# Optimization experiments

Measured on AMD Instinct MI355X. Metric: run time of the kernel, lower is better.

Reference implementation:

```python
import jax, jax.numpy as jnp
import numpy as np

NEG_INF = -1e30


def setup_inputs() -> dict:
    key = jax.random.key(0)
    k1, k2, k3, k4, k5, k6 = jax.random.split(key, 6)
    B, CL, QL, H = 16, 512, 64, 768
    c = jax.random.normal(k1, (B, CL, H), dtype=jnp.float32)
    q = jax.random.normal(k2, (B, QL, H), dtype=jnp.float32)
    c_mask = jax.random.randint(k3, (B, CL), 0, 2, dtype=jnp.int32)
    q_mask = jax.random.randint(k4, (B, QL), 0, 2, dtype=jnp.int32)
    W = jax.random.normal(k5, (H, H), dtype=jnp.float32) * (1.0 / np.sqrt(H))
    b = jax.random.normal(k6, (H,), dtype=jnp.float32) * 0.01
    return {"c": c, "q": q, "c_mask": c_mask, "q_mask": q_mask, "W": W, "b": b}


def reference(c, q, c_mask, q_mask, W, b):
    # c: [B, CL, H], q: [B, QL, H]
    cm = c_mask.astype(bool)[:, :, None]   # [B, CL, 1]
    qm = q_mask.astype(bool)[:, None, :]   # [B, 1, QL]
    # projected context then similarity matrix s: [B, CL, QL]
    cp = jnp.einsum('bch,dh->bcd', c, W) + b
    s = jnp.einsum('bcd,bqd->bcq', cp, q)
    # dual masked softmax (c2q over query dim, q2c over context dim)
    s1 = jax.nn.softmax(jnp.where(qm, s, NEG_INF), axis=2)  # [B, CL, QL]
    s2 = jax.nn.softmax(jnp.where(cm, s, NEG_INF), axis=1)  # [B, CL, QL]
    # a = s1 @ q : context-to-query attention
    a = jnp.einsum('bcq,bqh->bch', s1, q)
    # bvec = (s1 @ s2^T) @ c : query-to-context attention
    ss = jnp.einsum('bcq,bdq->bcd', s1, s2)  # [B, CL, CL]
    bvec = jnp.einsum('bcd,bdh->bch', ss, c)
    x = jnp.concatenate([c, a, c * a, c * bvec], axis=2)  # [B, CL, 4H]
    return x
```

## Files before the change

kernel.cpp:

```cpp
#include <hip/hip_runtime.h>
#include <math.h>


#define B_  16
#define CL_ 512
#define QL_ 64
#define H_  768
#define M_  (B_ * CL_)

typedef __attribute__((ext_vector_type(8))) short s8v;
typedef __attribute__((ext_vector_type(4))) float f4v;

__device__ __forceinline__ unsigned short bf16_rne(float x) {
    unsigned int u = __float_as_uint(x);
    u += 0x7fffu + ((u >> 16) & 1u);
    return (unsigned short)(u >> 16);
}
__device__ __forceinline__ float bf16_f(unsigned short h) {
    return __uint_as_float((unsigned int)h << 16);
}
__device__ __forceinline__ void split2(float x, unsigned short& h, unsigned short& l) {
    h = bf16_rne(x);
    l = bf16_rne(x - bf16_f(h));
}

__global__ __launch_bounds__(256) void k_u_beta(const float* __restrict__ q,
    const float* __restrict__ W, const float* __restrict__ bias,
    unsigned short* __restrict__ uh, unsigned short* __restrict__ ul,
    float* __restrict__ beta)
{
    if (blockIdx.x >= 192) {
        const int row = (blockIdx.x - 192) * 4 + (threadIdx.x >> 6);
        const int lane = threadIdx.x & 63;
        float p = 0.f;
        for (int d = lane; d < H_; d += 64) p = fmaf(bias[d], q[(size_t)row * H_ + d], p);
#pragma unroll
        for (int o = 32; o; o >>= 1) p += __shfl_xor(p, o);
        if (lane == 0) beta[row] = p;
        return;
    }
    __shared__ unsigned short Wh[64][40], Wl[64][40];
    const int m0 = (blockIdx.x & 15) * 64, n0 = (blockIdx.x >> 4) * 64;
    const int t = threadIdx.x, w = t >> 6, lane = t & 63;
    const int fm = lane & 15, quad = lane >> 4;
    const int mrow = m0 + w * 16 + fm;
    const int dd = t >> 3, hc = (t & 7) * 8;
    f4v acc[4];
#pragma unroll
    for (int j = 0; j < 4; ++j) acc[j] = (f4v){0.f, 0.f, 0.f, 0.f};
    for (int k0 = 0; k0 < H_; k0 += 32) {
        const float* wp = &W[(size_t)(k0 + dd) * H_ + n0 + hc];
        const float4 v0 = *(const float4*)wp, v1 = *(const float4*)(wp + 4);
        const float* ap = &q[(size_t)mrow * H_ + k0 + quad * 8];
        const float4 a0 = *(const float4*)ap, a1 = *(const float4*)(ap + 4);
        const float as[8] = {a0.x, a0.y, a0.z, a0.w, a1.x, a1.y, a1.z, a1.w};
        s8v fah, fal;
#pragma unroll
        for (int j = 0; j < 8; ++j) { unsigned short h, l; split2(as[j], h, l); fah[j] = (short)h; fal[j] = (short)l; }
        const float ws[8] = {v0.x, v0.y, v0.z, v0.w, v1.x, v1.y, v1.z, v1.w};
        __syncthreads();
#pragma unroll
        for (int j = 0; j < 8; ++j) {
            unsigned short h, l; split2(ws[j], h, l);
            Wh[hc + j][dd] = h; Wl[hc + j][dd] = l;
        }
        __syncthreads();
#pragma unroll
        for (int tn = 0; tn < 4; ++tn) {
            const s8v bh = *(const s8v*)&Wh[tn * 16 + fm][quad * 8];
            const s8v bl = *(const s8v*)&Wl[tn * 16 + fm][quad * 8];
            acc[tn] = __builtin_amdgcn_mfma_f32_16x16x32_bf16(fah, bh, acc[tn], 0, 0, 0);
            acc[tn] = __builtin_amdgcn_mfma_f32_16x16x32_bf16(fah, bl, acc[tn], 0, 0, 0);
            acc[tn] = __builtin_amdgcn_mfma_f32_16x16x32_bf16(fal, bh, acc[tn], 0, 0, 0);
        }
    }
#pragma unroll
    for (int tn = 0; tn < 4; ++tn) {
        const int col = n0 + tn * 16 + fm;
#pragma unroll
        for (int r = 0; r < 4; ++r) {
            const int row = m0 + w * 16 + quad * 4 + r;
            unsigned short h, l; split2(acc[tn][r], h, l);
            uh[(size_t)row * H_ + col] = h;
            ul[(size_t)row * H_ + col] = l;
        }
    }
}

__global__ __launch_bounds__(256) void k_s_sm(const float* __restrict__ c,
    const unsigned short* __restrict__ uh, const unsigned short* __restrict__ ul,
    const float* __restrict__ beta, const int* __restrict__ q_mask,
    float* __restrict__ s, unsigned short* __restrict__ s1)
{
    __shared__ float sL[32][65];
    const int m0 = blockIdx.x * 32;
    const int batch = m0 >> 9;
    const int t = threadIdx.x, w = t >> 6, lane = t & 63;
    const int fm = lane & 15, quad = lane >> 4;
    const int msub = (w >> 1) * 16, ntile0 = (w & 1) * 2;
    const int mrow = m0 + msub + fm;
    f4v acc[2];
    acc[0] = (f4v){0.f, 0.f, 0.f, 0.f}; acc[1] = acc[0];
    for (int k0 = 0; k0 < H_; k0 += 32) {
        const float* ap = &c[(size_t)mrow * H_ + k0 + quad * 8];
        const float4 a0 = *(const float4*)ap, a1 = *(const float4*)(ap + 4);
        const float xs[8] = {a0.x, a0.y, a0.z, a0.w, a1.x, a1.y, a1.z, a1.w};
        s8v fah, fal;
#pragma unroll
        for (int j = 0; j < 8; ++j) { unsigned short h, l; split2(xs[j], h, l); fah[j] = (short)h; fal[j] = (short)l; }
#pragma unroll
        for (int i = 0; i < 2; ++i) {
            const int tn = ntile0 + i;
            const size_t bo = (size_t)(batch * QL_ + tn * 16 + fm) * H_ + k0 + quad * 8;
            const s8v bh = *(const s8v*)&uh[bo];
            const s8v bl = *(const s8v*)&ul[bo];
            acc[i] = __builtin_amdgcn_mfma_f32_16x16x32_bf16(fah, bh, acc[i], 0, 0, 0);
            acc[i] = __builtin_amdgcn_mfma_f32_16x16x32_bf16(fah, bl, acc[i], 0, 0, 0);
            acc[i] = __builtin_amdgcn_mfma_f32_16x16x32_bf16(fal, bh, acc[i], 0, 0, 0);
        }
    }
#pragma unroll
    for (int i = 0; i < 2; ++i) {
        const int col = (ntile0 + i) * 16 + fm;
        const float bb = beta[batch * QL_ + col];
#pragma unroll
        for (int r = 0; r < 4; ++r) {
            const int lr = msub + quad * 4 + r;
            const float v = acc[i][r] + bb;
            s[(size_t)(m0 + lr) * QL_ + col] = v;
            sL[lr][col] = v;
        }
    }
    __syncthreads();
    const bool qm = q_mask[batch * QL_ + lane] != 0;
#pragma unroll
    for (int rr = 0; rr < 8; ++rr) {
        const int lr = w * 8 + rr;
        const float x = qm ? sL[lr][lane] : -1e30f;
        float mx = x;
#pragma unroll
        for (int o = 32; o; o >>= 1) mx = fmaxf(mx, __shfl_xor(mx, o));
        const float e = __expf(x - mx);
        float sm = e;
#pragma unroll
        for (int o = 32; o; o >>= 1) sm += __shfl_xor(sm, o);
        s1[(size_t)(m0 + lr) * QL_ + lane] = bf16_rne(e / sm);
    }
}

__global__ __launch_bounds__(256) void k_sm_cols(const float* __restrict__ s,
    const int* __restrict__ c_mask, unsigned short* __restrict__ s2t)
{
    __shared__ float red[4];
    const int b = blockIdx.x >> 6, qi = blockIdx.x & 63;
    const int t = threadIdx.x;
    const float* sb = s + (size_t)b * CL_ * QL_ + qi;
    const int* cm = c_mask + b * CL_;
    float x0 = cm[t] ? sb[(size_t)t * QL_] : -1e30f;
    float x1 = cm[t + 256] ? sb[(size_t)(t + 256) * QL_] : -1e30f;
    float m = fmaxf(x0, x1);
#pragma unroll
    for (int o = 32; o; o >>= 1) m = fmaxf(m, __shfl_xor(m, o));
    if ((t & 63) == 0) red[t >> 6] = m;
    __syncthreads();
    m = fmaxf(fmaxf(red[0], red[1]), fmaxf(red[2], red[3]));
    __syncthreads();
    float e0 = __expf(x0 - m), e1 = __expf(x1 - m);
    float sm = e0 + e1;
#pragma unroll
    for (int o = 32; o; o >>= 1) sm += __shfl_xor(sm, o);
    if ((t & 63) == 0) red[t >> 6] = sm;
    __syncthreads();
    sm = red[0] + red[1] + red[2] + red[3];
    float inv = 1.f / sm;
    unsigned short* o = s2t + ((size_t)b * QL_ + qi) * CL_;
    o[t]       = bf16_rne(e0 * inv);
    o[t + 256] = bf16_rne(e1 * inv);
}

__global__ __launch_bounds__(256) void k_tfin(const unsigned short* __restrict__ s2t,
    const unsigned short* __restrict__ s1, const float* __restrict__ q,
    const float* __restrict__ c, float* __restrict__ out)
{
    __shared__ unsigned short Bs[64][40];
    __shared__ unsigned short qT[64][72];
    __shared__ unsigned short tT[64][72];
    const int h0 = blockIdx.x * 64;
    const int c0 = blockIdx.y * 256;
    const int b  = blockIdx.z;
    const int t = threadIdx.x, w = t >> 6, lane = t & 63;
    const int fm = lane & 15, quad = lane >> 4;

    {
        const int r = t >> 4, c4 = (t & 15) * 4;
#pragma unroll
        for (int i = 0; i < 4; ++i) {
            const int qr = r + 16 * i;
            const float4 v = *(const float4*)&q[((size_t)b * QL_ + qr) * H_ + h0 + c4];
            qT[c4 + 0][qr] = bf16_rne(v.x);
            qT[c4 + 1][qr] = bf16_rne(v.y);
            qT[c4 + 2][qr] = bf16_rne(v.z);
            qT[c4 + 3][qr] = bf16_rne(v.w);
        }
    }

    {
        const int dd = t >> 3, hc = (t & 7) * 8;
        f4v acc[4];
#pragma unroll
        for (int j = 0; j < 4; ++j) acc[j] = (f4v){0.f, 0.f, 0.f, 0.f};
        for (int d0 = 0; d0 < CL_; d0 += 32) {
            const float* cp = &c[((size_t)b * CL_ + d0 + dd) * H_ + h0 + hc];
            const float4 v0 = *(const float4*)cp, v1 = *(const float4*)(cp + 4);
            const float xs[8] = {v0.x, v0.y, v0.z, v0.w, v1.x, v1.y, v1.z, v1.w};
            __syncthreads();
#pragma unroll
            for (int j = 0; j < 8; ++j) Bs[hc + j][dd] = bf16_rne(xs[j]);
            __syncthreads();
            const s8v fb = *(const s8v*)&Bs[w * 16 + fm][quad * 8];
#pragma unroll
            for (int tm = 0; tm < 4; ++tm) {
                const s8v fa = *(const s8v*)&s2t[((size_t)b * QL_ + tm * 16 + fm) * CL_ + d0 + quad * 8];
                acc[tm] = __builtin_amdgcn_mfma_f32_16x16x32_bf16(fa, fb, acc[tm], 0, 0, 0);
            }
        }
#pragma unroll
        for (int tm = 0; tm < 4; ++tm)
#pragma unroll
            for (int r = 0; r < 4; ++r)
                tT[w * 16 + fm][tm * 16 + quad * 4 + r] = bf16_rne(acc[tm][r]);
    }
    __syncthreads();

    const int cbase = c0 + w * 64;
    f4v aa[4][4], bb[4][4];
#pragma unroll
    for (int i = 0; i < 4; ++i)
#pragma unroll
        for (int j = 0; j < 4; ++j) { aa[i][j] = (f4v){0.f, 0.f, 0.f, 0.f}; bb[i][j] = aa[i][j]; }
#pragma unroll
    for (int ks = 0; ks < 2; ++ks) {
        s8v fa[4], fq[4], ft[4];
#pragma unroll
        for (int tm = 0; tm < 4; ++tm)
            fa[tm] = *(const s8v*)&s1[(size_t)(b * CL_ + cbase + tm * 16 + fm) * QL_ + ks * 32 + quad * 8];
#pragma unroll
        for (int tn = 0; tn < 4; ++tn) {
            fq[tn] = *(const s8v*)&qT[tn * 16 + fm][ks * 32 + quad * 8];
            ft[tn] = *(const s8v*)&tT[tn * 16 + fm][ks * 32 + quad * 8];
        }
#pragma unroll
        for (int tm = 0; tm < 4; ++tm)
#pragma unroll
            for (int tn = 0; tn < 4; ++tn) {
                aa[tm][tn] = __builtin_amdgcn_mfma_f32_16x16x32_bf16(fa[tm], fq[tn], aa[tm][tn], 0, 0, 0);
                bb[tm][tn] = __builtin_amdgcn_mfma_f32_16x16x32_bf16(fa[tm], ft[tn], bb[tm][tn], 0, 0, 0);
            }
    }
#pragma unroll
    for (int tm = 0; tm < 4; ++tm)
#pragma unroll
        for (int tn = 0; tn < 4; ++tn) {
            const int h = h0 + tn * 16 + fm;
#pragma unroll
            for (int r = 0; r < 4; ++r) {
                const int crow = cbase + tm * 16 + quad * 4 + r;
                const float cv = c[((size_t)b * CL_ + crow) * H_ + h];
                const float av = aa[tm][tn][r], bv = bb[tm][tn][r];
                float* ob = out + (size_t)(b * CL_ + crow) * (4 * H_);
                ob[h]           = cv;
                ob[H_ + h]      = av;
                ob[2 * H_ + h]  = cv * av;
                ob[3 * H_ + h]  = cv * bv;
            }
        }
}

extern "C" void kernel_launch(void* const* d_in, const int* in_sizes, int n_in,
                              void* d_out, int out_size, void* d_ws, size_t ws_size,
                              hipStream_t stream) {
    const float* c      = (const float*)d_in[0];
    const float* q      = (const float*)d_in[1];
    const int*   c_mask = (const int*)d_in[2];
    const int*   q_mask = (const int*)d_in[3];
    const float* W      = (const float*)d_in[4];
    const float* bias   = (const float*)d_in[5];
    float* out = (float*)d_out;

    char* base = (char*)d_ws;
    unsigned short* uh   = (unsigned short*)(base);
    unsigned short* ul   = (unsigned short*)(base + 1572864);
    float*          beta = (float*)(base + 3145728);
    float*          s    = (float*)(base + 3149824);
    unsigned short* s1   = (unsigned short*)(base + 5246976);
    unsigned short* s2t  = (unsigned short*)(base + 6295552);

    dim3 blk(256);
    k_u_beta <<<dim3(192 + 256),  blk, 0, stream>>>(q, W, bias, uh, ul, beta);
    k_s_sm   <<<dim3(256),        blk, 0, stream>>>(c, uh, ul, beta, q_mask, s, s1);
    k_sm_cols<<<dim3(B_ * QL_),   blk, 0, stream>>>(s, c_mask, s2t);
    k_tfin   <<<dim3(12, 2, B_),  blk, 0, stream>>>(s2t, s1, q, c, out);
}
```

Before: 220.2 us.

## Pre-split operands, split final kernel, and raise grid parallelism

```diff
diff --git a/kernel.cpp b/kernel.cpp
--- a/kernel.cpp
+++ b/kernel.cpp
@@ -24,8 +24,71 @@
     l = bf16_rne(x - bf16_f(h));
 }
 
-__global__ __launch_bounds__(256) void k_u_beta(const float* __restrict__ q,
-    const float* __restrict__ W, const float* __restrict__ bias,
+__global__ __launch_bounds__(256) void k_split(const float* __restrict__ W,
+    const float* __restrict__ q,
+    unsigned short* __restrict__ wth, unsigned short* __restrict__ wtl,
+    unsigned short* __restrict__ qh,  unsigned short* __restrict__ ql,
+    unsigned short* __restrict__ qt)
+{
+    __shared__ float tile[64][68];
+    const int t = threadIdx.x;
+    const int r = t >> 4, c4 = (t & 15) * 4;
+    if (blockIdx.x < 144) {
+        const int d0 = (blockIdx.x % 12) * 64, h0 = (blockIdx.x / 12) * 64;
+#pragma unroll
+        for (int i = 0; i < 4; ++i)
+            *(float4*)&tile[r + 16 * i][c4] = *(const float4*)&W[(size_t)(d0 + r + 16 * i) * H_ + h0 + c4];
+        __syncthreads();
+#pragma unroll
+        for (int i = 0; i < 4; ++i) {
+            const int hr = r + 16 * i;
+            ushort4 hh, ll;
+            split2(tile[c4 + 0][hr], hh.x, ll.x);
+            split2(tile[c4 + 1][hr], hh.y, ll.y);
+            split2(tile[c4 + 2][hr], hh.z, ll.z);
+            split2(tile[c4 + 3][hr], hh.w, ll.w);
+            *(ushort4*)&wth[(size_t)(h0 + hr) * H_ + d0 + c4] = hh;
+            *(ushort4*)&wtl[(size_t)(h0 + hr) * H_ + d0 + c4] = ll;
+        }
+    } else {
+        const int idx = blockIdx.x - 144;
+        const int m0 = (idx & 15) * 64, h0 = (idx >> 4) * 64;
+        float4 v[4];
+#pragma unroll
+        for (int i = 0; i < 4; ++i) {
+            v[i] = *(const float4*)&q[(size_t)(m0 + r + 16 * i) * H_ + h0 + c4];
+            *(float4*)&tile[r + 16 * i][c4] = v[i];
+        }
+        __syncthreads();
+#pragma unroll
+        for (int i = 0; i < 4; ++i) {
+            const int row = m0 + r + 16 * i;
+            ushort4 hh, ll;
+            split2(v[i].x, hh.x, ll.x);
+            split2(v[i].y, hh.y, ll.y);
+            split2(v[i].z, hh.z, ll.z);
+            split2(v[i].w, hh.w, ll.w);
+            *(ushort4*)&qh[(size_t)row * H_ + h0 + c4] = hh;
+            *(ushort4*)&ql[(size_t)row * H_ + h0 + c4] = ll;
+        }
+        const int b = idx & 15;
+#pragma unroll
+        for (int i = 0; i < 4; ++i) {
+            const int hr = r + 16 * i;
+            ushort4 hh;
+            hh.x = bf16_rne(tile[c4 + 0][hr]);
+            hh.y = bf16_rne(tile[c4 + 1][hr]);
+            hh.z = bf16_rne(tile[c4 + 2][hr]);
+            hh.w = bf16_rne(tile[c4 + 3][hr]);
+            *(ushort4*)&qt[((size_t)b * H_ + h0 + hr) * QL_ + c4] = hh;
+        }
+    }
+}
+
+__global__ __launch_bounds__(256) void k_u_beta(
+    const unsigned short* __restrict__ qh, const unsigned short* __restrict__ ql,
+    const unsigned short* __restrict__ wth, const unsigned short* __restrict__ wtl,
+    const float* __restrict__ q, const float* __restrict__ bias,
     unsigned short* __restrict__ uh, unsigned short* __restrict__ ul,
     float* __restrict__ beta)
 {
@@ -39,36 +102,22 @@
         if (lane == 0) beta[row] = p;
         return;
     }
-    __shared__ unsigned short Wh[64][40], Wl[64][40];
     const int m0 = (blockIdx.x & 15) * 64, n0 = (blockIdx.x >> 4) * 64;
     const int t = threadIdx.x, w = t >> 6, lane = t & 63;
     const int fm = lane & 15, quad = lane >> 4;
     const int mrow = m0 + w * 16 + fm;
-    const int dd = t >> 3, hc = (t & 7) * 8;
     f4v acc[4];
 #pragma unroll
     for (int j = 0; j < 4; ++j) acc[j] = (f4v){0.f, 0.f, 0.f, 0.f};
     for (int k0 = 0; k0 < H_; k0 += 32) {
-        const float* wp = &W[(size_t)(k0 + dd) * H_ + n0 + hc];
-        const float4 v0 = *(const float4*)wp, v1 = *(const float4*)(wp + 4);
-        const float* ap = &q[(size_t)mrow * H_ + k0 + quad * 8];
-        const float4 a0 = *(const float4*)ap, a1 = *(const float4*)(ap + 4);
-        const float as[8] = {a0.x, a0.y, a0.z, a0.w, a1.x, a1.y, a1.z, a1.w};
-        s8v fah, fal;
-#pragma unroll
-        for (int j = 0; j < 8; ++j) { unsigned short h, l; split2(as[j], h, l); fah[j] = (short)h; fal[j] = (short)l; }
-        const float ws[8] = {v0.x, v0.y, v0.z, v0.w, v1.x, v1.y, v1.z, v1.w};
-        __syncthreads();
-#pragma unroll
-        for (int j = 0; j < 8; ++j) {
-            unsigned short h, l; split2(ws[j], h, l);
-            Wh[hc + j][dd] = h; Wl[hc + j][dd] = l;
-        }
-        __syncthreads();
+        const size_t ao = (size_t)mrow * H_ + k0 + quad * 8;
+        const s8v fah = *(const s8v*)&qh[ao];
+        const s8v fal = *(const s8v*)&ql[ao];
 #pragma unroll
         for (int tn = 0; tn < 4; ++tn) {
-            const s8v bh = *(const s8v*)&Wh[tn * 16 + fm][quad * 8];
-            const s8v bl = *(const s8v*)&Wl[tn * 16 + fm][quad * 8];
+            const size_t bo = (size_t)(n0 + tn * 16 + fm) * H_ + k0 + quad * 8;
+            const s8v bh = *(const s8v*)&wth[bo];
+            const s8v bl = *(const s8v*)&wtl[bo];
             acc[tn] = __builtin_amdgcn_mfma_f32_16x16x32_bf16(fah, bh, acc[tn], 0, 0, 0);
             acc[tn] = __builtin_amdgcn_mfma_f32_16x16x32_bf16(fah, bl, acc[tn], 0, 0, 0);
             acc[tn] = __builtin_amdgcn_mfma_f32_16x16x32_bf16(fal, bh, acc[tn], 0, 0, 0);
@@ -92,50 +141,50 @@
     const float* __restrict__ beta, const int* __restrict__ q_mask,
     float* __restrict__ s, unsigned short* __restrict__ s1)
 {
-    __shared__ float sL[32][65];
-    const int m0 = blockIdx.x * 32;
+    __shared__ unsigned short chh[2][16][40], cll[2][16][40];
+    __shared__ float sL[16][65];
+    const int m0 = blockIdx.x * 16;
     const int batch = m0 >> 9;
     const int t = threadIdx.x, w = t >> 6, lane = t & 63;
     const int fm = lane & 15, quad = lane >> 4;
-    const int msub = (w >> 1) * 16, ntile0 = (w & 1) * 2;
-    const int mrow = m0 + msub + fm;
-    f4v acc[2];
-    acc[0] = (f4v){0.f, 0.f, 0.f, 0.f}; acc[1] = acc[0];
+    const int srow = t >> 4, skk = (t & 15) * 2;
+    f4v acc = (f4v){0.f, 0.f, 0.f, 0.f};
+
+    float2 v = *(const float2*)&c[(size_t)(m0 + srow) * H_ + skk];
+    int p = 0;
     for (int k0 = 0; k0 < H_; k0 += 32) {
-        const float* ap = &c[(size_t)mrow * H_ + k0 + quad * 8];
-        const float4 a0 = *(const float4*)ap, a1 = *(const float4*)(ap + 4);
-        const float xs[8] = {a0.x, a0.y, a0.z, a0.w, a1.x, a1.y, a1.z, a1.w};
-        s8v fah, fal;
-#pragma unroll
-        for (int j = 0; j < 8; ++j) { unsigned short h, l; split2(xs[j], h, l); fah[j] = (short)h; fal[j] = (short)l; }
-#pragma unroll
-        for (int i = 0; i < 2; ++i) {
-            const int tn = ntile0 + i;
-            const size_t bo = (size_t)(batch * QL_ + tn * 16 + fm) * H_ + k0 + quad * 8;
-            const s8v bh = *(const s8v*)&uh[bo];
-            const s8v bl = *(const s8v*)&ul[bo];
-            acc[i] = __builtin_amdgcn_mfma_f32_16x16x32_bf16(fah, bh, acc[i], 0, 0, 0);
-            acc[i] = __builtin_amdgcn_mfma_f32_16x16x32_bf16(fah, bl, acc[i], 0, 0, 0);
-            acc[i] = __builtin_amdgcn_mfma_f32_16x16x32_bf16(fal, bh, acc[i], 0, 0, 0);
-        }
-    }
-#pragma unroll
-    for (int i = 0; i < 2; ++i) {
-        const int col = (ntile0 + i) * 16 + fm;
+        unsigned short h0s, l0s, h1s, l1s;
+        split2(v.x, h0s, l0s); split2(v.y, h1s, l1s);
+        *(ushort2*)&chh[p][srow][skk] = make_ushort2(h0s, h1s);
+        *(ushort2*)&cll[p][srow][skk] = make_ushort2(l0s, l1s);
+        __syncthreads();
+        if (k0 + 32 < H_) v = *(const float2*)&c[(size_t)(m0 + srow) * H_ + k0 + 32 + skk];
+        const s8v fah = *(const s8v*)&chh[p][fm][quad * 8];
+        const s8v fal = *(const s8v*)&cll[p][fm][quad * 8];
+        const size_t bo = (size_t)(batch * QL_ + w * 16 + fm) * H_ + k0 + quad * 8;
+        const s8v bh = *(const s8v*)&uh[bo];
+        const s8v bl = *(const s8v*)&ul[bo];
+        acc = __builtin_amdgcn_mfma_f32_16x16x32_bf16(fah, bh, acc, 0, 0, 0);
+        acc = __builtin_amdgcn_mfma_f32_16x16x32_bf16(fah, bl, acc, 0, 0, 0);
+        acc = __builtin_amdgcn_mfma_f32_16x16x32_bf16(fal, bh, acc, 0, 0, 0);
+        p ^= 1;
+    }
+    {
+        const int col = w * 16 + fm;
         const float bb = beta[batch * QL_ + col];
 #pragma unroll
         for (int r = 0; r < 4; ++r) {
-            const int lr = msub + quad * 4 + r;
-            const float v = acc[i][r] + bb;
-            s[(size_t)(m0 + lr) * QL_ + col] = v;
-            sL[lr][col] = v;
+            const int lr = quad * 4 + r;
+            const float vv = acc[r] + bb;
+            sL[lr][col] = vv;
+            s[(size_t)(m0 + lr) * QL_ + col] = vv;
         }
     }
     __syncthreads();
     const bool qm = q_mask[batch * QL_ + lane] != 0;
 #pragma unroll
-    for (int rr = 0; rr < 8; ++rr) {
-        const int lr = w * 8 + rr;
+    for (int rr = 0; rr < 4; ++rr) {
+        const int lr = w * 4 + rr;
         const float x = qm ? sL[lr][lane] : -1e30f;
         float mx = x;
 #pragma unroll
@@ -178,79 +227,74 @@
     o[t + 256] = bf16_rne(e1 * inv);
 }
 
-__global__ __launch_bounds__(256) void k_tfin(const unsigned short* __restrict__ s2t,
-    const unsigned short* __restrict__ s1, const float* __restrict__ q,
+__global__ __launch_bounds__(256) void k_t(const unsigned short* __restrict__ s2t,
+    const float* __restrict__ c, unsigned short* __restrict__ tt)
+{
+    __shared__ unsigned short Bs[2][64][40];
+    const int h0 = blockIdx.x * 64, b = blockIdx.y;
+    const int t = threadIdx.x, w = t >> 6, lane = t & 63;
+    const int fm = lane & 15, quad = lane >> 4;
+    const int dd = t >> 3, hc = (t & 7) * 8;
+    f4v acc[4];
+#pragma unroll
+    for (int j = 0; j < 4; ++j) acc[j] = (f4v){0.f, 0.f, 0.f, 0.f};
+
+    const float* cp0 = &c[((size_t)b * CL_ + dd) * H_ + h0 + hc];
+    float4 v0 = *(const float4*)cp0, v1 = *(const float4*)(cp0 + 4);
+    int p = 0;
+    for (int d0 = 0; d0 < CL_; d0 += 32) {
+        const float xs[8] = {v0.x, v0.y, v0.z, v0.w, v1.x, v1.y, v1.z, v1.w};
+#pragma unroll
+        for (int j = 0; j < 8; ++j) Bs[p][hc + j][dd] = bf16_rne(xs[j]);
+        __syncthreads();
+        if (d0 + 32 < CL_) {
+            const float* cp = &c[((size_t)b * CL_ + d0 + 32 + dd) * H_ + h0 + hc];
+            v0 = *(const float4*)cp; v1 = *(const float4*)(cp + 4);
+        }
+        const s8v fb = *(const s8v*)&Bs[p][w * 16 + fm][quad * 8];
+#pragma unroll
+        for (int tm = 0; tm < 4; ++tm) {
+            const s8v fa = *(const s8v*)&s2t[((size_t)b * QL_ + tm * 16 + fm) * CL_ + d0 + quad * 8];
+            acc[tm] = __builtin_amdgcn_mfma_f32_16x16x32_bf16(fa, fb, acc[tm], 0, 0, 0);
+        }
+        p ^= 1;
+    }
+#pragma unroll
+    for (int tm = 0; tm < 4; ++tm)
+#pragma unroll
+        for (int r = 0; r < 4; ++r)
+            tt[((size_t)b * H_ + h0 + w * 16 + fm) * QL_ + tm * 16 + quad * 4 + r] = bf16_rne(acc[tm][r]);
+}
+
+__global__ __launch_bounds__(256) void k_fin(const unsigned short* __restrict__ s1,
+    const unsigned short* __restrict__ qt, const unsigned short* __restrict__ tt,
     const float* __restrict__ c, float* __restrict__ out)
 {
-    __shared__ unsigned short Bs[64][40];
-    __shared__ unsigned short qT[64][72];
-    __shared__ unsigned short tT[64][72];
     const int h0 = blockIdx.x * 64;
-    const int c0 = blockIdx.y * 256;
+    const int c0 = blockIdx.y * 128;
     const int b  = blockIdx.z;
     const int t = threadIdx.x, w = t >> 6, lane = t & 63;
     const int fm = lane & 15, quad = lane >> 4;
-
-    {
-        const int r = t >> 4, c4 = (t & 15) * 4;
-#pragma unroll
-        for (int i = 0; i < 4; ++i) {
-            const int qr = r + 16 * i;
-            const float4 v = *(const float4*)&q[((size_t)b * QL_ + qr) * H_ + h0 + c4];
-            qT[c4 + 0][qr] = bf16_rne(v.x);
-            qT[c4 + 1][qr] = bf16_rne(v.y);
-            qT[c4 + 2][qr] = bf16_rne(v.z);
-            qT[c4 + 3][qr] = bf16_rne(v.w);
-        }
-    }
-
-    {
-        const int dd = t >> 3, hc = (t & 7) * 8;
-        f4v acc[4];
-#pragma unroll
-        for (int j = 0; j < 4; ++j) acc[j] = (f4v){0.f, 0.f, 0.f, 0.f};
-        for (int d0 = 0; d0 < CL_; d0 += 32) {
-            const float* cp = &c[((size_t)b * CL_ + d0 + dd) * H_ + h0 + hc];
-            const float4 v0 = *(const float4*)cp, v1 = *(const float4*)(cp + 4);
-            const float xs[8] = {v0.x, v0.y, v0.z, v0.w, v1.x, v1.y, v1.z, v1.w};
-            __syncthreads();
-#pragma unroll
-            for (int j = 0; j < 8; ++j) Bs[hc + j][dd] = bf16_rne(xs[j]);
-            __syncthreads();
-            const s8v fb = *(const s8v*)&Bs[w * 16 + fm][quad * 8];
-#pragma unroll
-            for (int tm = 0; tm < 4; ++tm) {
-                const s8v fa = *(const s8v*)&s2t[((size_t)b * QL_ + tm * 16 + fm) * CL_ + d0 + quad * 8];
-                acc[tm] = __builtin_amdgcn_mfma_f32_16x16x32_bf16(fa, fb, acc[tm], 0, 0, 0);
-            }
-        }
-#pragma unroll
-        for (int tm = 0; tm < 4; ++tm)
-#pragma unroll
-            for (int r = 0; r < 4; ++r)
-                tT[w * 16 + fm][tm * 16 + quad * 4 + r] = bf16_rne(acc[tm][r]);
-    }
-    __syncthreads();
-
-    const int cbase = c0 + w * 64;
-    f4v aa[4][4], bb[4][4];
-#pragma unroll
-    for (int i = 0; i < 4; ++i)
+    const int cbase = c0 + w * 32;
+    f4v aa[2][4], bb[2][4];
+#pragma unroll
+    for (int i = 0; i < 2; ++i)
 #pragma unroll
         for (int j = 0; j < 4; ++j) { aa[i][j] = (f4v){0.f, 0.f, 0.f, 0.f}; bb[i][j] = aa[i][j]; }
 #pragma unroll
     for (int ks = 0; ks < 2; ++ks) {
-        s8v fa[4], fq[4], ft[4];
-#pragma unroll
-        for (int tm = 0; tm < 4; ++tm)
+        s8v fa[2], fq[4], ft[4];
+#pragma unroll
+        for (int tm = 0; tm < 2; ++tm)
             fa[tm] = *(const s8v*)&s1[(size_t)(b * CL_ + cbase + tm * 16 + fm) * QL_ + ks * 32 + quad * 8];
 #pragma unroll
         for (int tn = 0; tn < 4; ++tn) {
-            fq[tn] = *(const s8v*)&qT[tn * 16 + fm][ks * 32 + quad * 8];
-            ft[tn] = *(const s8v*)&tT[tn * 16 + fm][ks * 32 + quad * 8];
-        }
-#pragma unroll
-        for (int tm = 0; tm < 4; ++tm)
+            const size_t ro = ((size_t)b * H_ + h0 + tn * 16 + fm) * QL_ + ks * 32 + quad * 8;
+            fq[tn] = *(const s8v*)&qt[ro];
+            ft[tn] = *(const s8v*)&tt[ro];
+        }
+#pragma unroll
+        for (int tm = 0; tm < 2; ++tm)
 #pragma unroll
             for (int tn = 0; tn < 4; ++tn) {
                 aa[tm][tn] = __builtin_amdgcn_mfma_f32_16x16x32_bf16(fa[tm], fq[tn], aa[tm][tn], 0, 0, 0);
@@ -258,7 +302,7 @@
             }
     }
 #pragma unroll
-    for (int tm = 0; tm < 4; ++tm)
+    for (int tm = 0; tm < 2; ++tm)
 #pragma unroll
         for (int tn = 0; tn < 4; ++tn) {
             const int h = h0 + tn * 16 + fm;
@@ -288,16 +332,24 @@
     float* out = (float*)d_out;
 
     char* base = (char*)d_ws;
-    unsigned short* uh   = (unsigned short*)(base);
-    unsigned short* ul   = (unsigned short*)(base + 1572864);
-    float*          beta = (float*)(base + 3145728);
-    float*          s    = (float*)(base + 3149824);
-    unsigned short* s1   = (unsigned short*)(base + 5246976);
-    unsigned short* s2t  = (unsigned short*)(base + 6295552);
+    unsigned short* wth  = (unsigned short*)(base);
+    unsigned short* wtl  = (unsigned short*)(base + 1179648);
+    float*          s    = (float*)(base);
+    unsigned short* qh   = (unsigned short*)(base + 2359296);
+    unsigned short* ql   = (unsigned short*)(base + 3932160);
+    unsigned short* s1   = (unsigned short*)(base + 2359296);
+    unsigned short* s2t  = (unsigned short*)(base + 3407872);
+    unsigned short* qt   = (unsigned short*)(base + 5505024);
+    unsigned short* uh   = (unsigned short*)(base + 7077888);
+    unsigned short* ul   = (unsigned short*)(base + 8650752);
+    unsigned short* tt   = (unsigned short*)(base + 7077888);
+    float*          beta = (float*)(base + 10223616);
 
     dim3 blk(256);
-    k_u_beta <<<dim3(192 + 256),  blk, 0, stream>>>(q, W, bias, uh, ul, beta);
-    k_s_sm   <<<dim3(256),        blk, 0, stream>>>(c, uh, ul, beta, q_mask, s, s1);
+    k_split  <<<dim3(336),        blk, 0, stream>>>(W, q, wth, wtl, qh, ql, qt);
+    k_u_beta <<<dim3(192 + 256),  blk, 0, stream>>>(qh, ql, wth, wtl, q, bias, uh, ul, beta);
+    k_s_sm   <<<dim3(512),        blk, 0, stream>>>(c, uh, ul, beta, q_mask, s, s1);
     k_sm_cols<<<dim3(B_ * QL_),   blk, 0, stream>>>(s, c_mask, s2t);
-    k_tfin   <<<dim3(12, 2, B_),  blk, 0, stream>>>(s2t, s1, q, c, out);
-}
+    k_t      <<<dim3(12, B_),     blk, 0, stream>>>(s2t, c, tt);
+    k_fin    <<<dim3(12, 4, B_),  blk, 0, stream>>>(s1, qt, tt, c, out);
+}
```

After: 223.8 us. About the same (+1.6%).

## Fuse column softmax into final kernel and restructure similarity GEMM tiling

Applied to the files above, without the earlier changes.

```diff
diff --git a/kernel.cpp b/kernel.cpp
--- a/kernel.cpp
+++ b/kernel.cpp
@@ -90,52 +90,51 @@
 __global__ __launch_bounds__(256) void k_s_sm(const float* __restrict__ c,
     const unsigned short* __restrict__ uh, const unsigned short* __restrict__ ul,
     const float* __restrict__ beta, const int* __restrict__ q_mask,
-    float* __restrict__ s, unsigned short* __restrict__ s1)
+    float* __restrict__ sT, unsigned short* __restrict__ s1)
 {
-    __shared__ float sL[32][65];
-    const int m0 = blockIdx.x * 32;
+    __shared__ unsigned short chh[2][16][40], cll[2][16][40];
+    __shared__ float sL[16][65];
+    const int m0 = blockIdx.x * 16;
     const int batch = m0 >> 9;
+    const int cloc = m0 & (CL_ - 1);
     const int t = threadIdx.x, w = t >> 6, lane = t & 63;
     const int fm = lane & 15, quad = lane >> 4;
-    const int msub = (w >> 1) * 16, ntile0 = (w & 1) * 2;
-    const int mrow = m0 + msub + fm;
-    f4v acc[2];
-    acc[0] = (f4v){0.f, 0.f, 0.f, 0.f}; acc[1] = acc[0];
+    const int srow = t >> 4, skk = (t & 15) * 2;
+    f4v acc = (f4v){0.f, 0.f, 0.f, 0.f};
+
+    float2 v = *(const float2*)&c[(size_t)(m0 + srow) * H_ + skk];
+    int p = 0;
     for (int k0 = 0; k0 < H_; k0 += 32) {
-        const float* ap = &c[(size_t)mrow * H_ + k0 + quad * 8];
-        const float4 a0 = *(const float4*)ap, a1 = *(const float4*)(ap + 4);
-        const float xs[8] = {a0.x, a0.y, a0.z, a0.w, a1.x, a1.y, a1.z, a1.w};
-        s8v fah, fal;
-#pragma unroll
-        for (int j = 0; j < 8; ++j) { unsigned short h, l; split2(xs[j], h, l); fah[j] = (short)h; fal[j] = (short)l; }
-#pragma unroll
-        for (int i = 0; i < 2; ++i) {
-            const int tn = ntile0 + i;
-            const size_t bo = (size_t)(batch * QL_ + tn * 16 + fm) * H_ + k0 + quad * 8;
-            const s8v bh = *(const s8v*)&uh[bo];
-            const s8v bl = *(const s8v*)&ul[bo];
-            acc[i] = __builtin_amdgcn_mfma_f32_16x16x32_bf16(fah, bh, acc[i], 0, 0, 0);
-            acc[i] = __builtin_amdgcn_mfma_f32_16x16x32_bf16(fah, bl, acc[i], 0, 0, 0);
-            acc[i] = __builtin_amdgcn_mfma_f32_16x16x32_bf16(fal, bh, acc[i], 0, 0, 0);
-        }
-    }
-#pragma unroll
-    for (int i = 0; i < 2; ++i) {
-        const int col = (ntile0 + i) * 16 + fm;
+        unsigned short h0s, l0s, h1s, l1s;
+        split2(v.x, h0s, l0s); split2(v.y, h1s, l1s);
+        *(ushort2*)&chh[p][srow][skk] = make_ushort2(h0s, h1s);
+        *(ushort2*)&cll[p][srow][skk] = make_ushort2(l0s, l1s);
+        __syncthreads();
+        if (k0 + 32 < H_) v = *(const float2*)&c[(size_t)(m0 + srow) * H_ + k0 + 32 + skk];
+        const s8v fah = *(const s8v*)&chh[p][fm][quad * 8];
+        const s8v fal = *(const s8v*)&cll[p][fm][quad * 8];
+        const size_t bo = (size_t)(batch * QL_ + w * 16 + fm) * H_ + k0 + quad * 8;
+        const s8v bh = *(const s8v*)&uh[bo];
+        const s8v bl = *(const s8v*)&ul[bo];
+        acc = __builtin_amdgcn_mfma_f32_16x16x32_bf16(fah, bh, acc, 0, 0, 0);
+        acc = __builtin_amdgcn_mfma_f32_16x16x32_bf16(fah, bl, acc, 0, 0, 0);
+        acc = __builtin_amdgcn_mfma_f32_16x16x32_bf16(fal, bh, acc, 0, 0, 0);
+        p ^= 1;
+    }
+    {
+        const int col = w * 16 + fm;
         const float bb = beta[batch * QL_ + col];
 #pragma unroll
         for (int r = 0; r < 4; ++r) {
-            const int lr = msub + quad * 4 + r;
-            const float v = acc[i][r] + bb;
-            s[(size_t)(m0 + lr) * QL_ + col] = v;
-            sL[lr][col] = v;
+            const int lr = quad * 4 + r;
+            sL[lr][col] = acc[r] + bb;
         }
     }
     __syncthreads();
     const bool qm = q_mask[batch * QL_ + lane] != 0;
 #pragma unroll
-    for (int rr = 0; rr < 8; ++rr) {
-        const int lr = w * 8 + rr;
+    for (int rr = 0; rr < 4; ++rr) {
+        const int lr = w * 4 + rr;
         const float x = qm ? sL[lr][lane] : -1e30f;
         float mx = x;
 #pragma unroll
@@ -146,50 +145,62 @@
         for (int o = 32; o; o >>= 1) sm += __shfl_xor(sm, o);
         s1[(size_t)(m0 + lr) * QL_ + lane] = bf16_rne(e / sm);
     }
-}
-
-__global__ __launch_bounds__(256) void k_sm_cols(const float* __restrict__ s,
-    const int* __restrict__ c_mask, unsigned short* __restrict__ s2t)
+    {
+        const int qq = t >> 2, c4o = (t & 3) * 4;
+        float4 ov;
+        ov.x = sL[c4o + 0][qq];
+        ov.y = sL[c4o + 1][qq];
+        ov.z = sL[c4o + 2][qq];
+        ov.w = sL[c4o + 3][qq];
+        *(float4*)&sT[((size_t)batch * QL_ + qq) * CL_ + cloc + c4o] = ov;
+    }
+}
+
+__global__ __launch_bounds__(256) void k_tfin3(const float* __restrict__ sT,
+    const unsigned short* __restrict__ s1, const float* __restrict__ q,
+    const float* __restrict__ c, const int* __restrict__ c_mask,
+    float* __restrict__ out)
 {
-    __shared__ float red[4];
-    const int b = blockIdx.x >> 6, qi = blockIdx.x & 63;
-    const int t = threadIdx.x;
-    const float* sb = s + (size_t)b * CL_ * QL_ + qi;
-    const int* cm = c_mask + b * CL_;
-    float x0 = cm[t] ? sb[(size_t)t * QL_] : -1e30f;
-    float x1 = cm[t + 256] ? sb[(size_t)(t + 256) * QL_] : -1e30f;
-    float m = fmaxf(x0, x1);
-#pragma unroll
-    for (int o = 32; o; o >>= 1) m = fmaxf(m, __shfl_xor(m, o));
-    if ((t & 63) == 0) red[t >> 6] = m;
-    __syncthreads();
-    m = fmaxf(fmaxf(red[0], red[1]), fmaxf(red[2], red[3]));
-    __syncthreads();
-    float e0 = __expf(x0 - m), e1 = __expf(x1 - m);
-    float sm = e0 + e1;
-#pragma unroll
-    for (int o = 32; o; o >>= 1) sm += __shfl_xor(sm, o);
-    if ((t & 63) == 0) red[t >> 6] = sm;
-    __syncthreads();
-    sm = red[0] + red[1] + red[2] + red[3];
-    float inv = 1.f / sm;
-    unsigned short* o = s2t + ((size_t)b * QL_ + qi) * CL_;
-    o[t]       = bf16_rne(e0 * inv);
-    o[t + 256] = bf16_rne(e1 * inv);
-}
-
-__global__ __launch_bounds__(256) void k_tfin(const unsigned short* __restrict__ s2t,
-    const unsigned short* __restrict__ s1, const float* __restrict__ q,
-    const float* __restrict__ c, float* __restrict__ out)
-{
-    __shared__ unsigned short Bs[64][40];
+    __shared__ unsigned short s2L[64 * 512];
     __shared__ unsigned short qT[64][72];
     __shared__ unsigned short tT[64][72];
+    __shared__ unsigned short Bs[2][64][40];
     const int h0 = blockIdx.x * 64;
-    const int c0 = blockIdx.y * 256;
-    const int b  = blockIdx.z;
+    const int b  = blockIdx.y;
     const int t = threadIdx.x, w = t >> 6, lane = t & 63;
     const int fm = lane & 15, quad = lane >> 4;
+
+    {
+        const int cbase8 = lane * 8;
+        int cm8[8];
+#pragma unroll
+        for (int j = 0; j < 8; ++j) cm8[j] = c_mask[b * CL_ + cbase8 + j];
+        const float* stb = sT + (size_t)b * QL_ * CL_;
+        for (int qi = 0; qi < 16; ++qi) {
+            const int qq = w * 16 + qi;
+            const float* sr = stb + (size_t)qq * CL_ + cbase8;
+            const float4 v0 = *(const float4*)sr, v1 = *(const float4*)(sr + 4);
+            float x[8] = {v0.x, v0.y, v0.z, v0.w, v1.x, v1.y, v1.z, v1.w};
+#pragma unroll
+            for (int j = 0; j < 8; ++j) x[j] = cm8[j] ? x[j] : -1e30f;
+            float m = x[0];
+#pragma unroll
+            for (int j = 1; j < 8; ++j) m = fmaxf(m, x[j]);
+#pragma unroll
+            for (int o = 32; o; o >>= 1) m = fmaxf(m, __shfl_xor(m, o));
+            float e[8], sm = 0.f;
+#pragma unroll
+            for (int j = 0; j < 8; ++j) { e[j] = __expf(x[j] - m); sm += e[j]; }
+#pragma unroll
+            for (int o = 32; o; o >>= 1) sm += __shfl_xor(sm, o);
+            const float inv = 1.f / sm;
+            s8v sv;
+#pragma unroll
+            for (int j = 0; j < 8; ++j) sv[j] = (short)bf16_rne(e[j] * inv);
+            const int boff = ((qq * 512 + cbase8) * 2) ^ ((qq & 7) << 4);
+            *(s8v*)((char*)s2L + boff) = sv;
+        }
+    }
 
     {
         const int r = t >> 4, c4 = (t & 15) * 4;
@@ -209,20 +220,26 @@
         f4v acc[4];
 #pragma unroll
         for (int j = 0; j < 4; ++j) acc[j] = (f4v){0.f, 0.f, 0.f, 0.f};
+        const float* cp0 = &c[((size_t)b * CL_ + dd) * H_ + h0 + hc];
+        float4 v0 = *(const float4*)cp0, v1 = *(const float4*)(cp0 + 4);
+        int p = 0;
         for (int d0 = 0; d0 < CL_; d0 += 32) {
-            const float* cp = &c[((size_t)b * CL_ + d0 + dd) * H_ + h0 + hc];
-            const float4 v0 = *(const float4*)cp, v1 = *(const float4*)(cp + 4);
             const float xs[8] = {v0.x, v0.y, v0.z, v0.w, v1.x, v1.y, v1.z, v1.w};
+#pragma unroll
+            for (int j = 0; j < 8; ++j) Bs[p][hc + j][dd] = bf16_rne(xs[j]);
             __syncthreads();
-#pragma unroll
-            for (int j = 0; j < 8; ++j) Bs[hc + j][dd] = bf16_rne(xs[j]);
-            __syncthreads();
-            const s8v fb = *(const s8v*)&Bs[w * 16 + fm][quad * 8];
+            if (d0 + 32 < CL_) {
+                const float* cp = &c[((size_t)b * CL_ + d0 + 32 + dd) * H_ + h0 + hc];
+                v0 = *(const float4*)cp; v1 = *(const float4*)(cp + 4);
+            }
+            const s8v fb = *(const s8v*)&Bs[p][w * 16 + fm][quad * 8];
 #pragma unroll
             for (int tm = 0; tm < 4; ++tm) {
-                const s8v fa = *(const s8v*)&s2t[((size_t)b * QL_ + tm * 16 + fm) * CL_ + d0 + quad * 8];
+                const int boff = (((tm * 16 + fm) * 512 + d0 + quad * 8) * 2) ^ ((fm & 7) << 4);
+                const s8v fa = *(const s8v*)((const char*)s2L + boff);
                 acc[tm] = __builtin_amdgcn_mfma_f32_16x16x32_bf16(fa, fb, acc[tm], 0, 0, 0);
             }
+            p ^= 1;
         }
 #pragma unroll
         for (int tm = 0; tm < 4; ++tm)
@@ -232,48 +249,50 @@
     }
     __syncthreads();
 
-    const int cbase = c0 + w * 64;
-    f4v aa[4][4], bb[4][4];
-#pragma unroll
-    for (int i = 0; i < 4; ++i)
-#pragma unroll
-        for (int j = 0; j < 4; ++j) { aa[i][j] = (f4v){0.f, 0.f, 0.f, 0.f}; bb[i][j] = aa[i][j]; }
-#pragma unroll
-    for (int ks = 0; ks < 2; ++ks) {
-        s8v fa[4], fq[4], ft[4];
+    for (int cc = 0; cc < 2; ++cc) {
+        const int cbase = cc * 256 + w * 64;
+        f4v aa[4][4], bb[4][4];
+#pragma unroll
+        for (int i = 0; i < 4; ++i)
+#pragma unroll
+            for (int j = 0; j < 4; ++j) { aa[i][j] = (f4v){0.f, 0.f, 0.f, 0.f}; bb[i][j] = aa[i][j]; }
+#pragma unroll
+        for (int ks = 0; ks < 2; ++ks) {
+            s8v fa[4], fq[4], ft[4];
+#pragma unroll
+            for (int tm = 0; tm < 4; ++tm)
+                fa[tm] = *(const s8v*)&s1[(size_t)(b * CL_ + cbase + tm * 16 + fm) * QL_ + ks * 32 + quad * 8];
+#pragma unroll
+            for (int tn = 0; tn < 4; ++tn) {
+                fq[tn] = *(const s8v*)&qT[tn * 16 + fm][ks * 32 + quad * 8];
+                ft[tn] = *(const s8v*)&tT[tn * 16 + fm][ks * 32 + quad * 8];
+            }
+#pragma unroll
+            for (int tm = 0; tm < 4; ++tm)
+#pragma unroll
+                for (int tn = 0; tn < 4; ++tn) {
+                    aa[tm][tn] = __builtin_amdgcn_mfma_f32_16x16x32_bf16(fa[tm], fq[tn], aa[tm][tn], 0, 0, 0);
+                    bb[tm][tn] = __builtin_amdgcn_mfma_f32_16x16x32_bf16(fa[tm], ft[tn], bb[tm][tn], 0, 0, 0);
+                }
+        }
 #pragma unroll
         for (int tm = 0; tm < 4; ++tm)
-            fa[tm] = *(const s8v*)&s1[(size_t)(b * CL_ + cbase + tm * 16 + fm) * QL_ + ks * 32 + quad * 8];
-#pragma unroll
-        for (int tn = 0; tn < 4; ++tn) {
-            fq[tn] = *(const s8v*)&qT[tn * 16 + fm][ks * 32 + quad * 8];
-            ft[tn] = *(const s8v*)&tT[tn * 16 + fm][ks * 32 + quad * 8];
-        }
-#pragma unroll
-        for (int tm = 0; tm < 4; ++tm)
 #pragma unroll
             for (int tn = 0; tn < 4; ++tn) {
-                aa[tm][tn] = __builtin_amdgcn_mfma_f32_16x16x32_bf16(fa[tm], fq[tn], aa[tm][tn], 0, 0, 0);
-                bb[tm][tn] = __builtin_amdgcn_mfma_f32_16x16x32_bf16(fa[tm], ft[tn], bb[tm][tn], 0, 0, 0);
+                const int h = h0 + tn * 16 + fm;
+#pragma unroll
+                for (int r = 0; r < 4; ++r) {
+                    const int crow = cbase + tm * 16 + quad * 4 + r;
+                    const float cv = c[((size_t)b * CL_ + crow) * H_ + h];
+                    const float av = aa[tm][tn][r], bv = bb[tm][tn][r];
+                    float* ob = out + (size_t)(b * CL_ + crow) * (4 * H_);
+                    ob[h]           = cv;
+                    ob[H_ + h]      = av;
+                    ob[2 * H_ + h]  = cv * av;
+                    ob[3 * H_ + h]  = cv * bv;
+                }
             }
     }
-#pragma unroll
-    for (int tm = 0; tm < 4; ++tm)
-#pragma unroll
-        for (int tn = 0; tn < 4; ++tn) {
-            const int h = h0 + tn * 16 + fm;
-#pragma unroll
-            for (int r = 0; r < 4; ++r) {
-                const int crow = cbase + tm * 16 + quad * 4 + r;
-                const float cv = c[((size_t)b * CL_ + crow) * H_ + h];
-                const float av = aa[tm][tn][r], bv = bb[tm][tn][r];
-                float* ob = out + (size_t)(b * CL_ + crow) * (4 * H_);
-                ob[h]           = cv;
-                ob[H_ + h]      = av;
-                ob[2 * H_ + h]  = cv * av;
-                ob[3 * H_ + h]  = cv * bv;
-            }
-        }
 }
 
 extern "C" void kernel_launch(void* const* d_in, const int* in_sizes, int n_in,
@@ -291,13 +310,11 @@
     unsigned short* uh   = (unsigned short*)(base);
     unsigned short* ul   = (unsigned short*)(base + 1572864);
     float*          beta = (float*)(base + 3145728);
-    float*          s    = (float*)(base + 3149824);
+    float*          sT   = (float*)(base + 3149824);
     unsigned short* s1   = (unsigned short*)(base + 5246976);
-    unsigned short* s2t  = (unsigned short*)(base + 6295552);
 
     dim3 blk(256);
     k_u_beta <<<dim3(192 + 256),  blk, 0, stream>>>(q, W, bias, uh, ul, beta);
-    k_s_sm   <<<dim3(256),        blk, 0, stream>>>(c, uh, ul, beta, q_mask, s, s1);
-    k_sm_cols<<<dim3(B_ * QL_),   blk, 0, stream>>>(s, c_mask, s2t);
-    k_tfin   <<<dim3(12, 2, B_),  blk, 0, stream>>>(s2t, s1, q, c, out);
-}
+    k_s_sm   <<<dim3(512),        blk, 0, stream>>>(c, uh, ul, beta, q_mask, sT, s1);
+    k_tfin3  <<<dim3(12, 16),     blk, 0, stream>>>(sT, s1, q, c, c_mask, out);
+}
```

Result: faster. 207.5 us (-5.8%).
